# Kernel optimization log

Hardware: AMD Instinct MI355X
Metric: run time of the kernel (lower is better)

## Reference

```python
import jax, jax.numpy as jnp
import numpy as np

ROUTING_ITERS = 3
SQUASH_EPS = 1e-7


def squash(s):
    # squash along last axis (capsule vector dim); equals squash_axis=-2 in the
    # original [B,1,Nout,D,1] layout since we carry s as [B,Nout,D].
    sq = jnp.sum(s * s, axis=-1, keepdims=True)
    scale = sq / (1.0 + sq) / jnp.sqrt(sq + SQUASH_EPS)
    return scale * s


def setup_inputs() -> dict:
    key = jax.random.key(0)
    k1, k2 = jax.random.split(key)
    B, Nin, Din = 128, 1152, 8
    Nout, D = 10, 16
    x = jax.random.normal(k1, (B, Nin, Din), dtype=jnp.float32)
    # glorot_uniform over fan_in=Din, fan_out=D for the [D,Din] transform
    limit = np.sqrt(6.0 / (Din + D)).astype(np.float32)
    W = jax.random.uniform(k2, (Nin, Nout, D, Din), dtype=jnp.float32,
                           minval=-limit, maxval=limit)
    bias = jnp.zeros((Nout, D), dtype=jnp.float32)
    return {"x": x, "W": W, "bias": bias}


def reference(x, W, bias):
    # u_hat[b,i,j,d] = sum_k W[i,j,d,k] * x[b,i,k]   -> [B, Nin, Nout, D]
    u_hat = jnp.einsum('ijdk,bik->bijd', W, x)
    B, Nin, Nout, D = u_hat.shape
    b = jnp.zeros((B, Nin, Nout), dtype=u_hat.dtype)  # routing logits
    v = None
    for it in range(ROUTING_ITERS):
        c = jax.nn.softmax(b, axis=2)                       # over output capsules
        s = jnp.einsum('bij,bijd->bjd', c, u_hat) + bias    # weighted sum + bias
        v = squash(s)                                       # [B, Nout, D]
        if it < ROUTING_ITERS - 1:
            b = b + jnp.einsum('bijd,bjd->bij', u_hat, v)   # agreement update
    return v
```

## Files before the change

kernel.cpp:

```cpp
#include <hip/hip_runtime.h>

#define TI 8
#define NCH (1152 / TI)
#define SCELLS (128 * 10 * 16)
#define PADX 68

template<int CTRL>
__device__ __forceinline__ float dpp_add(float v) {
    int o = __builtin_amdgcn_update_dpp(0, __float_as_int(v), CTRL, 0xf, 0xf, true);
    return v + __int_as_float(o);
}
__device__ __forceinline__ float swz_xor4(float v) {
    return __int_as_float(__builtin_amdgcn_ds_swizzle(__float_as_int(v), 0x101F));
}

template<int ITER>
__global__ __launch_bounds__(256, 2)
void caps_pass(const float* __restrict__ x, const float* __restrict__ W,
               const float* __restrict__ vin, float* __restrict__ p)
{
    __shared__ float sW[TI * 1280];
    __shared__ float sX[32 * PADX];

    const int ic  = blockIdx.x;
    const int bq  = blockIdx.y;
    const int i0  = ic * TI;
    const int b0  = bq * 32;
    const int tid = threadIdx.x;

    {
        const float4* Wg  = reinterpret_cast<const float4*>(W + (size_t)i0 * 1280);
        float4*       sWf = reinterpret_cast<float4*>(sW);
        for (int t = tid; t < TI * 320; t += 256) {
            int il = t / 320, S = t % 320;
            int Sp = S ^ ((S >> 3) & 1);
            sWf[il * 320 + Sp] = Wg[t];
        }
    }
    {
        float4* sXf = reinterpret_cast<float4*>(sX);
        for (int t = tid; t < 32 * 16; t += 256) {
            int r = t / 16, c = t % 16;
            sXf[r * 17 + c] = *reinterpret_cast<const float4*>(
                x + (size_t)(b0 + r) * 9216 + i0 * 8 + c * 4);
        }
    }
    __syncthreads();

    const int dl = (tid & 3) | ((tid >> 1) & 4);
    const int jh = (tid >> 2) & 1;
    const int bL = ((tid >> 4) & 15) * 2;

    float vr[2][5][2];
    if (ITER >= 1) {
#pragma unroll
        for (int bb = 0; bb < 2; ++bb)
#pragma unroll
            for (int jj = 0; jj < 5; ++jj)
#pragma unroll
                for (int h = 0; h < 2; ++h)
                    vr[bb][jj][h] = vin[(size_t)(b0 + bL + bb) * 160 +
                                        (jh * 5 + jj) * 16 + dl + 8 * h];
    }

    float s_acc[2][5][2];
#pragma unroll
    for (int bb = 0; bb < 2; ++bb)
#pragma unroll
        for (int jj = 0; jj < 5; ++jj)
#pragma unroll
            for (int h = 0; h < 2; ++h) s_acc[bb][jj][h] = 0.f;

#pragma unroll 1
    for (int il = 0; il < TI; ++il) {
        float xr[2][8];
#pragma unroll
        for (int bb = 0; bb < 2; ++bb) {
            const float4* px = reinterpret_cast<const float4*>(&sX[(bL + bb) * PADX + il * 8]);
            float4 a = px[0], b = px[1];
            xr[bb][0] = a.x; xr[bb][1] = a.y; xr[bb][2] = a.z; xr[bb][3] = a.w;
            xr[bb][4] = b.x; xr[bb][5] = b.y; xr[bb][6] = b.z; xr[bb][7] = b.w;
        }
        float u[2][5][2];
#pragma unroll
        for (int jj = 0; jj < 5; ++jj) {
#pragma unroll
            for (int h = 0; h < 2; ++h) {
                const int j  = jh * 5 + jj;
                const int d  = dl + 8 * h;
                const int S0 = j * 32 + d * 2;
                const int sw = (S0 >> 3) & 1;
                const float4 w0 = *reinterpret_cast<const float4*>(
                    &sW[il * 1280 + (S0 ^ sw) * 4]);
                const float4 w1 = *reinterpret_cast<const float4*>(
                    &sW[il * 1280 + ((S0 + 1) ^ sw) * 4]);
#pragma unroll
                for (int bb = 0; bb < 2; ++bb) {
                    float acc = w0.x * xr[bb][0];
                    acc = fmaf(w0.y, xr[bb][1], acc);
                    acc = fmaf(w0.z, xr[bb][2], acc);
                    acc = fmaf(w0.w, xr[bb][3], acc);
                    acc = fmaf(w1.x, xr[bb][4], acc);
                    acc = fmaf(w1.y, xr[bb][5], acc);
                    acc = fmaf(w1.z, xr[bb][6], acc);
                    acc = fmaf(w1.w, xr[bb][7], acc);
                    u[bb][jj][h] = acc;
                }
            }
        }

        float c[2][5];
        if (ITER == 0) {
#pragma unroll
            for (int bb = 0; bb < 2; ++bb)
#pragma unroll
                for (int jj = 0; jj < 5; ++jj) c[bb][jj] = 0.1f;
        } else {
            float lp[2][5];
#pragma unroll
            for (int bb = 0; bb < 2; ++bb)
#pragma unroll
                for (int jj = 0; jj < 5; ++jj) {
                    float t = fmaf(u[bb][jj][1], vr[bb][jj][1],
                                   u[bb][jj][0] * vr[bb][jj][0]);
                    t = dpp_add<0xB1>(t);
                    t = dpp_add<0x4E>(t);
                    t = dpp_add<0x128>(t);
                    lp[bb][jj] = t;
                }
#pragma unroll
            for (int bb = 0; bb < 2; ++bb) {
                float mx = fmaxf(fmaxf(fmaxf(lp[bb][0], lp[bb][1]),
                                       fmaxf(lp[bb][2], lp[bb][3])), lp[bb][4]);
                mx = fmaxf(mx, swz_xor4(mx));
                float e0 = __expf(lp[bb][0] - mx);
                float e1 = __expf(lp[bb][1] - mx);
                float e2 = __expf(lp[bb][2] - mx);
                float e3 = __expf(lp[bb][3] - mx);
                float e4 = __expf(lp[bb][4] - mx);
                float sm = e0 + e1 + e2 + e3 + e4;
                sm += swz_xor4(sm);
                float inv = 1.0f / sm;
                c[bb][0] = e0 * inv; c[bb][1] = e1 * inv; c[bb][2] = e2 * inv;
                c[bb][3] = e3 * inv; c[bb][4] = e4 * inv;
            }
        }
#pragma unroll
        for (int bb = 0; bb < 2; ++bb)
#pragma unroll
            for (int jj = 0; jj < 5; ++jj)
#pragma unroll
                for (int h = 0; h < 2; ++h)
                    s_acc[bb][jj][h] = fmaf(c[bb][jj], u[bb][jj][h], s_acc[bb][jj][h]);
    }

    float* pp = p + (size_t)ic * SCELLS;
#pragma unroll
    for (int bb = 0; bb < 2; ++bb)
#pragma unroll
        for (int jj = 0; jj < 5; ++jj)
#pragma unroll
            for (int h = 0; h < 2; ++h)
                pp[(b0 + bL + bb) * 160 + (jh * 5 + jj) * 16 + dl + 8 * h] =
                    s_acc[bb][jj][h];
}

template<int MODE>
__global__ __launch_bounds__(256)
void caps_squash(const float* __restrict__ p, const float* __restrict__ bias,
                 const float* __restrict__ v_prev, float* __restrict__ v_out)
{
    __shared__ float part[4][64];
    const int tid  = threadIdx.x;
    const int w    = tid >> 6;
    const int lane = tid & 63;
    const int c    = blockIdx.x * 64 + lane;

    float acc = 0.f;
    const float* pw = p + (size_t)(w * (NCH / 4)) * SCELLS + c;
#pragma unroll 6
    for (int t = 0; t < NCH / 4; ++t) acc += pw[(size_t)t * SCELLS];
    part[w][lane] = acc;
    __syncthreads();

    if (tid < 64) {
        const int cc = blockIdx.x * 64 + tid;
        float tot = part[0][tid] + part[1][tid] + part[2][tid] + part[3][tid]
                  + bias[cc % 160];

        float sq = tot * tot;
        sq += __shfl_xor(sq, 1, 64);
        sq += __shfl_xor(sq, 2, 64);
        sq += __shfl_xor(sq, 4, 64);
        sq += __shfl_xor(sq, 8, 64);

        float scale = sq / ((1.0f + sq) * sqrtf(sq + 1e-7f));
        float v = tot * scale;

        if (MODE == 1) v += v_prev[cc];
        v_out[cc] = v;
    }
}

extern "C" void kernel_launch(void* const* d_in, const int* in_sizes, int n_in,
                              void* d_out, int out_size, void* d_ws, size_t ws_size,
                              hipStream_t stream)
{
    const float* x    = (const float*)d_in[0];
    const float* W    = (const float*)d_in[1];
    const float* bias = (const float*)d_in[2];
    float* out = (float*)d_out;

    float* p  = (float*)d_ws;
    float* vA = p + (size_t)NCH * SCELLS;
    float* vB = vA + SCELLS;

    dim3 pgrid(NCH, 4);
    dim3 sgrid(SCELLS / 64);
    caps_pass<0><<<pgrid, 256, 0, stream>>>(x, W, nullptr, p);
    caps_squash<0><<<sgrid, 256, 0, stream>>>(p, bias, nullptr, vA);
    caps_pass<1><<<pgrid, 256, 0, stream>>>(x, W, vA, p);
    caps_squash<1><<<sgrid, 256, 0, stream>>>(p, bias, vA, vB);
    caps_pass<2><<<pgrid, 256, 0, stream>>>(x, W, vB, p);
    caps_squash<2><<<sgrid, 256, 0, stream>>>(p, bias, nullptr, out);
}
```

Measured before the change: 136.4 us.

## Fuse squash reduction into pass kernel via last-arriving-block atomic counter

Removes the separate squash kernels by having each pass block bump a per-batch-quarter atomic counter after writing partials. The last 16 arriving blocks for each quarter then reduce all 144 partial chunks for a slice of cells, apply bias and squash, and write v. This cuts three kernel launches and their launch gaps. In exchange the final reduction runs on only 64 blocks, each thread summing 144 strided values serially, and a memset is added. The reduction also relies on threadfence visibility of partials written by other blocks.

Result: slower. 409.6 us (+200.3%).

```diff
diff --git a/kernel.cpp b/kernel.cpp
--- a/kernel.cpp
+++ b/kernel.cpp
@@ -4,6 +4,7 @@
 #define NCH (1152 / TI)
 #define SCELLS (128 * 10 * 16)
 #define PADX 68
+#define LASTN 16
 
 template<int CTRL>
 __device__ __forceinline__ float dpp_add(float v) {
@@ -17,10 +18,13 @@
 template<int ITER>
 __global__ __launch_bounds__(256, 2)
 void caps_pass(const float* __restrict__ x, const float* __restrict__ W,
-               const float* __restrict__ vin, float* __restrict__ p)
+               const float* __restrict__ bias, float* __restrict__ p,
+               float* __restrict__ vA, float* __restrict__ vB,
+               float* __restrict__ out, int* __restrict__ cnt)
 {
     __shared__ float sW[TI * 1280];
     __shared__ float sX[32 * PADX];
+    __shared__ int   s_arrival;
 
     const int ic  = blockIdx.x;
     const int bq  = blockIdx.y;
@@ -51,6 +55,7 @@
     const int jh = (tid >> 2) & 1;
     const int bL = ((tid >> 4) & 15) * 2;
 
+    const float* __restrict__ vin = (ITER == 1) ? vA : vB;
     float vr[2][5][2];
     if (ITER >= 1) {
 #pragma unroll
@@ -154,51 +159,49 @@
                     s_acc[bb][jj][h] = fmaf(c[bb][jj], u[bb][jj][h], s_acc[bb][jj][h]);
     }
 
-    float* pp = p + (size_t)ic * SCELLS;
-#pragma unroll
-    for (int bb = 0; bb < 2; ++bb)
-#pragma unroll
-        for (int jj = 0; jj < 5; ++jj)
-#pragma unroll
-            for (int h = 0; h < 2; ++h)
-                pp[(b0 + bL + bb) * 160 + (jh * 5 + jj) * 16 + dl + 8 * h] =
-                    s_acc[bb][jj][h];
-}
-
-template<int MODE>
-__global__ __launch_bounds__(256)
-void caps_squash(const float* __restrict__ p, const float* __restrict__ bias,
-                 const float* __restrict__ v_prev, float* __restrict__ v_out)
-{
-    __shared__ float part[4][64];
-    const int tid  = threadIdx.x;
-    const int w    = tid >> 6;
-    const int lane = tid & 63;
-    const int c    = blockIdx.x * 64 + lane;
-
-    float acc = 0.f;
-    const float* pw = p + (size_t)(w * (NCH / 4)) * SCELLS + c;
-#pragma unroll 6
-    for (int t = 0; t < NCH / 4; ++t) acc += pw[(size_t)t * SCELLS];
-    part[w][lane] = acc;
+    {
+        float* pp = p + (size_t)ic * SCELLS;
+#pragma unroll
+        for (int bb = 0; bb < 2; ++bb)
+#pragma unroll
+            for (int jj = 0; jj < 5; ++jj)
+#pragma unroll
+                for (int h = 0; h < 2; ++h)
+                    pp[(b0 + bL + bb) * 160 + (jh * 5 + jj) * 16 + dl + 8 * h] =
+                        s_acc[bb][jj][h];
+    }
+
     __syncthreads();
-
-    if (tid < 64) {
-        const int cc = blockIdx.x * 64 + tid;
-        float tot = part[0][tid] + part[1][tid] + part[2][tid] + part[3][tid]
-                  + bias[cc % 160];
-
-        float sq = tot * tot;
+    __threadfence();
+    if (tid == 0) s_arrival = atomicAdd(&cnt[bq], 1);
+    __syncthreads();
+    const int a = s_arrival;
+    if (a < NCH - LASTN) return;
+
+    const int slice = a - (NCH - LASTN);
+    const int base  = bq * 5120 + slice * 320;
+#pragma unroll 1
+    for (int r = 0; r < 2; ++r) {
+        const int t = tid + r * 256;
+        if (t >= 320) break;
+        const int cell = base + t;
+        float acc = bias[cell % 160];
+        const float* pw = p + cell;
+#pragma unroll 8
+        for (int icr = 0; icr < NCH; ++icr) acc += pw[(size_t)icr * SCELLS];
+
+        float sq = acc * acc;
         sq += __shfl_xor(sq, 1, 64);
         sq += __shfl_xor(sq, 2, 64);
         sq += __shfl_xor(sq, 4, 64);
         sq += __shfl_xor(sq, 8, 64);
 
         float scale = sq / ((1.0f + sq) * sqrtf(sq + 1e-7f));
-        float v = tot * scale;
-
-        if (MODE == 1) v += v_prev[cc];
-        v_out[cc] = v;
+        float v = acc * scale;
+
+        if (ITER == 1) v += vA[cell];
+        float* dst = (ITER == 0) ? vA : ((ITER == 1) ? vB : out);
+        dst[cell] = v;
     }
 }
 
@@ -214,13 +217,12 @@
     float* p  = (float*)d_ws;
     float* vA = p + (size_t)NCH * SCELLS;
     float* vB = vA + SCELLS;
+    int*   cnt = (int*)(vB + SCELLS);
+
+    hipMemsetAsync(cnt, 0, 12 * sizeof(int), stream);
 
     dim3 pgrid(NCH, 4);
-    dim3 sgrid(SCELLS / 64);
-    caps_pass<0><<<pgrid, 256, 0, stream>>>(x, W, nullptr, p);
-    caps_squash<0><<<sgrid, 256, 0, stream>>>(p, bias, nullptr, vA);
-    caps_pass<1><<<pgrid, 256, 0, stream>>>(x, W, vA, p);
-    caps_squash<1><<<sgrid, 256, 0, stream>>>(p, bias, vA, vB);
-    caps_pass<2><<<pgrid, 256, 0, stream>>>(x, W, vB, p);
-    caps_squash<2><<<sgrid, 256, 0, stream>>>(p, bias, nullptr, out);
-}
+    caps_pass<0><<<pgrid, 256, 0, stream>>>(x, W, bias, p, vA, vB, out, cnt + 0);
+    caps_pass<1><<<pgrid, 256, 0, stream>>>(x, W, bias, p, vA, vB, out, cnt + 4);
+    caps_pass<2><<<pgrid, 256, 0, stream>>>(x, W, bias, p, vA, vB, out, cnt + 8);
+}
```
